# Kernel optimization log

Measured on AMD Instinct MI355X. Metric: run time of the kernel, lower is better.

## Reference

```python
import jax, jax.numpy as jnp
import numpy as np

E = 64      # routed experts
K = 2       # top-k
CAP = 1024


def setup_inputs() -> dict:
    key = jax.random.key(0)
    ks = jax.random.split(key, 5)
    S, B, D, DFF = 2048, 4, 1024, 1408
    x = jax.random.normal(ks[0], (S, B, D), jnp.float32)
    Wg = jax.random.normal(ks[1], (D, E), jnp.float32) * 0.02
    W1 = jax.random.normal(ks[2], (E, D, DFF), jnp.float32) * 0.02
    W3 = jax.random.normal(ks[3], (E, D, DFF), jnp.float32) * 0.02
    W2 = jax.random.normal(ks[4], (E, DFF, D), jnp.float32) * 0.02
    return {"x": x, "Wg": Wg, "W1": W1, "W3": W3, "W2": W2}


def _moe(x, Wg, W1, W3, W2):
    S, B, D = x.shape
    tokens = jnp.transpose(x, (1, 0, 2)).reshape(-1, D)       # [T, D], T = B*S
    T = tokens.shape[0]

    # --- gate: softmax -> top-k, renormalize, aux loss (GShard-style) ---
    logits = tokens @ Wg                                       # [T, E]
    probs = jax.nn.softmax(logits, axis=-1)
    topk_w, topk_idx = jax.lax.top_k(probs, K)                 # [T, K]
    topk_w = topk_w / jnp.sum(topk_w, axis=-1, keepdims=True)
    me = jnp.mean(probs, axis=0)                               # [E] mean prob
    ce = jnp.mean(jax.nn.one_hot(topk_idx, E, dtype=jnp.float32).sum(1), axis=0) / K
    l_aux = E * jnp.sum(me * ce)

    # --- dispatch: per-pair slot within its expert via cumsum of one-hots ---
    flat_e = topk_idx.reshape(-1)                              # [T*K]
    oh = jax.nn.one_hot(flat_e, E, dtype=jnp.int32)            # [T*K, E]
    pos = jnp.cumsum(oh, axis=0) - 1                           # slot per expert
    slot = jnp.take_along_axis(pos, flat_e[:, None], axis=1)[:, 0]  # [T*K]
    keep = slot < CAP
    slot = jnp.where(keep, slot, 0)
    xr = jnp.repeat(tokens, K, axis=0)                         # [T*K, D]
    xr = jnp.where(keep[:, None], xr, 0.0)
    buf = jnp.zeros((E, CAP, D), x.dtype).at[flat_e, slot].add(xr)  # [E, C, D]

    # --- grouped expert FFN: SiLU-gated MLP per expert ---
    h = jax.nn.silu(jnp.einsum('ecd,edf->ecf', buf, W1)) * jnp.einsum('ecd,edf->ecf', buf, W3)
    eo = jnp.einsum('ecf,efd->ecd', h, W2)                     # [E, C, D]

    # --- combine: gather back, weight by gate probs, sum over k ---
    gathered = eo[flat_e, slot] * keep[:, None].astype(x.dtype)  # [T*K, D]
    combined = jnp.sum(gathered.reshape(T, K, D) * topk_w[..., None], axis=1)
    y = jnp.transpose(combined.reshape(B, S, D), (1, 0, 2))    # back to [S, B, D]
    return y, l_aux


def reference(x, Wg, W1, W3, W2):
    return _moe(x, Wg, W1, W3, W2)
```

## Files before the change

kernel.cpp:

```cpp
#include <hip/hip_runtime.h>
#include <hip/hip_bf16.h>


#define S_ 2048
#define B_ 4
#define D_ 1024
#define DFF_ 1408
#define E_ 64
#define T_ 8192
#define KTOP_ 2
#define NPAIR_ (T_*KTOP_)
#define PAD_ 384
#define ROWS_ (E_*PAD_)

#define BM 128
#define BN 64
#define BK 32

typedef __attribute__((ext_vector_type(8))) short short8;
typedef __attribute__((ext_vector_type(4))) short s16x4;
typedef __attribute__((ext_vector_type(4))) float f32x4;
typedef __attribute__((ext_vector_type(4))) unsigned short us4;

constexpr size_t OFF_PROBS  = 0;
constexpr size_t OFF_PE     = OFF_PROBS + (size_t)T_*E_*4;
constexpr size_t OFF_PW     = OFF_PE + (size_t)NPAIR_*4;
constexpr size_t OFF_COUNTS = OFF_PW + (size_t)NPAIR_*4;
constexpr size_t OFF_CURSOR = OFF_COUNTS + 256;
constexpr size_t OFF_MESUM  = OFF_CURSOR + 256;
constexpr size_t OFF_ROWTOK = OFF_MESUM + 256;
constexpr size_t OFF_ROWW   = OFF_ROWTOK + (size_t)ROWS_*4;
constexpr size_t OFF_XBUF   = OFF_ROWW + (size_t)ROWS_*4;
constexpr size_t OFF_H      = OFF_XBUF + (size_t)ROWS_*D_*2;

__device__ __forceinline__ short f2bfs(float f) {
  union { __hip_bfloat16 h; short s; } u;
  u.h = __float2bfloat16(f);
  return u.s;
}

__device__ __forceinline__ int SWZ(int g) { return g ^ (((g >> 4) & 3) << 1); }

#define BAR() do {                                   \
    __builtin_amdgcn_sched_barrier(0);               \
    __builtin_amdgcn_s_barrier();                    \
    __builtin_amdgcn_sched_barrier(0);               \
  } while (0)
#define WAIT_LGKM0() asm volatile("s_waitcnt lgkmcnt(0)" ::: "memory")

__device__ __forceinline__ float softmax64(float acc, int lane) {
  float m = acc;
  for (int o = 32; o; o >>= 1) m = fmaxf(m, __shfl_xor(m, o));
  float p = expf(acc - m);
  float s = p;
  for (int o = 32; o; o >>= 1) s += __shfl_xor(s, o);
  return p / s;
}

__device__ __forceinline__ void topk_write(float p, int t, int lane,
    float* __restrict__ probs, int* __restrict__ pe, float* __restrict__ pw,
    int* __restrict__ counts) {
  probs[(size_t)t * E_ + lane] = p;
  float v1 = p; int i1 = lane;
  for (int o = 32; o; o >>= 1) {
    float ov = __shfl_xor(v1, o); int oi = __shfl_xor(i1, o);
    if (ov > v1 || (ov == v1 && oi < i1)) { v1 = ov; i1 = oi; }
  }
  float v2 = (lane == i1) ? -1.f : p; int i2 = lane;
  for (int o = 32; o; o >>= 1) {
    float ov = __shfl_xor(v2, o); int oi = __shfl_xor(i2, o);
    if (ov > v2 || (ov == v2 && oi < i2)) { v2 = ov; i2 = oi; }
  }
  if (lane == 0) {
    float wsum = v1 + v2;
    pe[2 * t]     = i1; pw[2 * t]     = v1 / wsum;
    pe[2 * t + 1] = i2; pw[2 * t + 1] = v2 / wsum;
    atomicAdd(&counts[i1], 1);
    atomicAdd(&counts[i2], 1);
  }
}

__global__ __launch_bounds__(256) void gate_kernel(
    const float* __restrict__ x, const float* __restrict__ Wg,
    float* __restrict__ probs, int* __restrict__ pe, float* __restrict__ pw,
    int* __restrict__ counts) {
  int t0 = blockIdx.x * 8;
  int tid = threadIdx.x;
  int lane = tid & 63, wv = tid >> 6;
  __shared__ float tk[8][D_];
  for (int u = tid; u < 8 * (D_ / 4); u += 256) {
    int r = u >> 8, c4 = u & 255;
    int t = t0 + r;
    int b = t >> 11, s = t & (S_ - 1);
    ((float4*)tk[r])[c4] = ((const float4*)(x + (size_t)(s * B_ + b) * D_))[c4];
  }
  __syncthreads();
  const float* tkA = tk[2 * wv];
  const float* tkB = tk[2 * wv + 1];
  float acc0 = 0.f, acc1 = 0.f;
  #pragma unroll 8
  for (int d = 0; d < D_; ++d) {
    float w = Wg[(size_t)d * E_ + lane];
    acc0 += tkA[d] * w;
    acc1 += tkB[d] * w;
  }
  int ta = t0 + 2 * wv, tb = ta + 1;
  float p0 = softmax64(acc0, lane);
  float p1 = softmax64(acc1, lane);
  topk_write(p0, ta, lane, probs, pe, pw, counts);
  topk_write(p1, tb, lane, probs, pe, pw, counts);
}

__global__ __launch_bounds__(256) void me_kernel(const float* __restrict__ probs,
                                                 float* __restrict__ mesum) {
  int e = blockIdx.x, tid = threadIdx.x;
  float a = 0.f;
  for (int t = tid; t < T_; t += 256) a += probs[(size_t)t * E_ + e];
  __shared__ float red[256];
  red[tid] = a; __syncthreads();
  for (int s = 128; s; s >>= 1) {
    if (tid < s) red[tid] += red[tid + s];
    __syncthreads();
  }
  if (tid == 0) mesum[e] = red[0];
}

__global__ __launch_bounds__(64) void finalize_kernel(
    const int* __restrict__ counts, const float* __restrict__ mesum,
    float* __restrict__ laux_out) {
  int lane = threadIdx.x;
  float contrib = (mesum[lane] / (float)T_) * ((float)counts[lane] / (float)(T_ * KTOP_));
  for (int o = 32; o; o >>= 1) contrib += __shfl_xor(contrib, o);
  if (lane == 0) laux_out[0] = (float)E_ * contrib;
}

__global__ __launch_bounds__(64) void scatter_kernel(
    const float* __restrict__ x, const int* __restrict__ pe, const float* __restrict__ pw,
    int* __restrict__ cursor, int* __restrict__ rowtok, float* __restrict__ roww,
    unsigned short* __restrict__ xbufO) {
  int p = blockIdx.x;
  int lane = threadIdx.x;
  __shared__ int srow;
  __shared__ int sexp;
  if (lane == 0) {
    int e = pe[p];
    int slot = atomicAdd(&cursor[e], 1);
    int row = (slot < PAD_) ? slot : -1;
    if (row >= 0) { rowtok[e * PAD_ + row] = p >> 1; roww[e * PAD_ + row] = pw[p]; }
    srow = row; sexp = e;
  }
  __syncthreads();
  int m = srow;
  if (m < 0) return;
  int e = sexp;
  int t = p >> 1;
  int b = t >> 11, s = t & (S_ - 1);
  const float4* src = (const float4*)(x + (size_t)(s * B_ + b) * D_);
  unsigned short* dstE = xbufO + (size_t)e * D_ * PAD_;
  #pragma unroll
  for (int oo = 0; oo < 2; ++oo) {
    int o = lane + oo * 64;
    float4 lo = src[o * 2], hi = src[o * 2 + 1];
    short8 g;
    g[0] = f2bfs(lo.x); g[1] = f2bfs(lo.y); g[2] = f2bfs(lo.z); g[3] = f2bfs(lo.w);
    g[4] = f2bfs(hi.x); g[5] = f2bfs(hi.y); g[6] = f2bfs(hi.z); g[7] = f2bfs(hi.w);
    *(short8*)(dstE + ((size_t)o * PAD_ + m) * 8) = g;
  }
}

__global__ __launch_bounds__(256, 3) void ffn1_kernel(
    const unsigned short* __restrict__ xbufO, const float* __restrict__ W1,
    const float* __restrict__ W3, const int* __restrict__ counts,
    unsigned short* __restrict__ hO) {
  int bid = blockIdx.x;
  int r = bid & 7, u = bid >> 3;
  int mb = u % 3; int v = u / 3;
  int ni = v % 22; int eg = v / 22;
  int e = eg * 8 + r;
  int n0 = ni * BN;
  int m0 = mb * BM;
  int Me = min(counts[e], PAD_);
  if (m0 >= Me) return;

  const unsigned short* AO = xbufO + (size_t)e * D_ * PAD_;
  const float* B1p = W1 + (size_t)e * D_ * DFF_ + n0;
  const float* B3p = W3 + (size_t)e * D_ * DFF_ + n0;
  unsigned short* hE = hO + (size_t)e * PAD_ * DFF_;

  __shared__ short B1s[2 * BK * BN];
  __shared__ short B3s[2 * BK * BN];
  __shared__ short Hb[BM * BN];

  int tid = threadIdx.x;
  int lane = tid & 63;
  int wv = tid >> 6, wr = wv >> 1, wc = wv & 1;

  int msel = tid >> 7;
  int t7 = tid & 127;
  int col4 = t7 & 15;
  int krow0 = (t7 >> 4) << 2;
  const float* qB = (msel ? B3p : B1p) + (size_t)krow0 * DFF_ + col4 * 4;
  char* Bdst = (char*)(msel ? B3s : B1s);
  int kseg = krow0 >> 3, khalf8 = ((krow0 >> 2) & 1) << 3;
  int sub = col4 >> 2;
  int boffc[4];
  #pragma unroll
  for (int cc = 0; cc < 4; ++cc)
    boffc[cc] = (sub << 10) + (SWZ((kseg << 4) + ((col4 & 3) * 4 + cc)) << 4) + khalf8;

  const unsigned short* qa =
      AO + (((size_t)(lane >> 4)) * PAD_ + m0 + (wr << 6) + (lane & 15)) * 8;

  short8 afE[4], afO[4];
  f32x4 fBE[4], fBO[4];
  f32x4 acc1[4][2] = {};
  f32x4 acc3[4][2] = {};

#define F1_ALOAD(SET) do {                                               \
    _Pragma("unroll")                                                    \
    for (int mi = 0; mi < 4; ++mi)                                       \
      af##SET[mi] = *(const short8*)(qa + mi * 128);                     \
    qa += (size_t)4 * PAD_ * 8;                                          \
  } while (0)

#define F1_BLOAD(SET) do {                                               \
    _Pragma("unroll")                                                    \
    for (int j = 0; j < 4; ++j)                                          \
      fB##SET[j] = *(const f32x4*)(qB + (size_t)j * DFF_);               \
    qB += (size_t)BK * DFF_;                                             \
  } while (0)

#define F1_BWRITE(SET, BUF) do {                                         \
    _Pragma("unroll")                                                    \
    for (int cc = 0; cc < 4; ++cc) {                                     \
      s16x4 w;                                                           \
      _Pragma("unroll")                                                  \
      for (int j = 0; j < 4; ++j) w[j] = f2bfs(fB##SET[j][cc]);          \
      *(s16x4*)(Bdst + (BUF)*4096 + boffc[cc]) = w;                      \
    }                                                                    \
  } while (0)

#define F1_MFMA(BUF, SET) do {                                           \
    int lsw = SWZ(lane) << 4;                                            \
    __builtin_amdgcn_s_setprio(1);                                       \
    _Pragma("unroll")                                                    \
    for (int q = 0; q < 2; ++q) {                                        \
      short8 bf1 = *(const short8*)((char*)B1s + (BUF)*4096 + (((wc << 1) + q) << 10) + lsw); \
      short8 bf3 = *(const short8*)((char*)B3s + (BUF)*4096 + (((wc << 1) + q) << 10) + lsw); \
      _Pragma("unroll")                                                  \
      for (int mi = 0; mi < 4; ++mi) {                                   \
        acc1[mi][q] = __builtin_amdgcn_mfma_f32_16x16x32_bf16(af##SET[mi], bf1, acc1[mi][q], 0, 0, 0); \
        acc3[mi][q] = __builtin_amdgcn_mfma_f32_16x16x32_bf16(af##SET[mi], bf3, acc3[mi][q], 0, 0, 0); \
      }                                                                  \
    }                                                                    \
    __builtin_amdgcn_s_setprio(0);                                       \
  } while (0)

  F1_ALOAD(E); F1_BLOAD(E);
  F1_ALOAD(O); F1_BLOAD(O);
  for (int it = 0; it < 15; ++it) {
    F1_BWRITE(E, 0); WAIT_LGKM0(); BAR();
    F1_MFMA(0, E);
    BAR();
    F1_ALOAD(E); F1_BLOAD(E);
    F1_BWRITE(O, 1); WAIT_LGKM0(); BAR();
    F1_MFMA(1, O);
    BAR();
    F1_ALOAD(O); F1_BLOAD(O);
  }
  F1_BWRITE(E, 0); WAIT_LGKM0(); BAR(); F1_MFMA(0, E); BAR();
  F1_BWRITE(O, 1); WAIT_LGKM0(); BAR(); F1_MFMA(1, O);

  __syncthreads();
  int lr = (lane >> 4) << 2, lc = lane & 15;
  #pragma unroll
  for (int mi = 0; mi < 4; ++mi) {
    #pragma unroll
    for (int j = 0; j < 4; ++j) {
      int m = ((wr << 2) + mi) * 16 + lr + j;
      #pragma unroll
      for (int q = 0; q < 2; ++q) {
        int c = (wc << 5) + (q << 4) + lc;
        float a = acc1[mi][q][j];
        float gt = a / (1.f + __expf(-a));
        Hb[((c >> 3) * BM + m) * 8 + (c & 7)] = f2bfs(gt * acc3[mi][q][j]);
      }
    }
  }
  __syncthreads();
  int co = tid >> 5, ml0 = (tid & 31) << 2;
  size_t fo = (size_t)(n0 >> 3) + co;
  #pragma unroll
  for (int i = 0; i < 4; ++i) {
    int ml = ml0 + i;
    short8 vq = *(const short8*)(Hb + ((size_t)co * BM + ml) * 8);
    *(short8*)(hE + (fo * PAD_ + m0 + ml) * 8) = vq;
  }
}

__global__ __launch_bounds__(256, 4) void ffn2_kernel(
    const unsigned short* __restrict__ hO, const float* __restrict__ W2,
    const int* __restrict__ counts, const int* __restrict__ rowtok,
    const float* __restrict__ roww, float* __restrict__ y) {
  int bid = blockIdx.x;
  int r = bid & 7, u = bid >> 3;
  int mb = u % 3; int v = u / 3;
  int ni = v % 16; int eg = v / 16;
  int e = eg * 8 + r;
  int n0 = ni * BN;
  int m0 = mb * BM;
  int Me = min(counts[e], PAD_);
  if (m0 >= Me) return;

  const unsigned short* AO = hO + (size_t)e * PAD_ * DFF_;
  const float* Bw = W2 + (size_t)e * DFF_ * D_ + n0;

  __shared__ short Bs[2 * BK * BN];

  int tid = threadIdx.x;
  int lane = tid & 63;
  int wv = tid >> 6, wr = wv >> 1, wc = wv & 1;

  int bstage = (tid < 128);
  int t7 = tid & 127;
  int col4 = t7 & 15;
  int krow0 = (t7 >> 4) << 2;
  const float* qB = Bw + (size_t)krow0 * D_ + col4 * 4;
  int kseg = krow0 >> 3, khalf8 = ((krow0 >> 2) & 1) << 3;
  int sub = col4 >> 2;
  int boffc[4];
  #pragma unroll
  for (int cc = 0; cc < 4; ++cc)
    boffc[cc] = (sub << 10) + (SWZ((kseg << 4) + ((col4 & 3) * 4 + cc)) << 4) + khalf8;

  const unsigned short* qa =
      AO + (((size_t)(lane >> 4)) * PAD_ + m0 + (wr << 6) + (lane & 15)) * 8;

  short8 afE[4], afO[4];
  f32x4 fBE[4], fBO[4];
  f32x4 acc[4][2] = {};

#define F2_ALOAD(SET) do {                                               \
    _Pragma("unroll")                                                    \
    for (int mi = 0; mi < 4; ++mi)                                       \
      af##SET[mi] = *(const short8*)(qa + mi * 128);                     \
    qa += (size_t)4 * PAD_ * 8;                                          \
  } while (0)

#define F2_BLOAD(SET) do {                                               \
    if (bstage) {                                                        \
      _Pragma("unroll")                                                  \
      for (int j = 0; j < 4; ++j)                                        \
        fB##SET[j] = *(const f32x4*)(qB + (size_t)j * D_);               \
    }                                                                    \
    qB += (size_t)BK * D_;                                               \
  } while (0)

#define F2_BWRITE(SET, BUF) do {                                         \
    if (bstage) {                                                        \
      _Pragma("unroll")                                                  \
      for (int cc = 0; cc < 4; ++cc) {                                   \
        s16x4 w;                                                         \
        _Pragma("unroll")                                                \
        for (int j = 0; j < 4; ++j) w[j] = f2bfs(fB##SET[j][cc]);        \
        *(s16x4*)((char*)Bs + (BUF)*4096 + boffc[cc]) = w;               \
      }                                                                  \
    }                                                                    \
  } while (0)

#define F2_MFMA(BUF, SET) do {                                           \
    int lsw = SWZ(lane) << 4;                                            \
    __builtin_amdgcn_s_setprio(1);                                       \
    _Pragma("unroll")                                                    \
    for (int q = 0; q < 2; ++q) {                                        \
      short8 bfr = *(const short8*)((char*)Bs + (BUF)*4096 + (((wc << 1) + q) << 10) + lsw); \
      _Pragma("unroll")                                                  \
      for (int mi = 0; mi < 4; ++mi)                                     \
        acc[mi][q] = __builtin_amdgcn_mfma_f32_16x16x32_bf16(af##SET[mi], bfr, acc[mi][q], 0, 0, 0); \
    }                                                                    \
    __builtin_amdgcn_s_setprio(0);                                       \
  } while (0)

  F2_ALOAD(E); F2_BLOAD(E);
  F2_ALOAD(O); F2_BLOAD(O);
  for (int it = 0; it < 21; ++it) {
    F2_BWRITE(E, 0); WAIT_LGKM0(); BAR();
    F2_MFMA(0, E);
    BAR();
    F2_ALOAD(E); F2_BLOAD(E);
    F2_BWRITE(O, 1); WAIT_LGKM0(); BAR();
    F2_MFMA(1, O);
    BAR();
    F2_ALOAD(O); F2_BLOAD(O);
  }
  F2_BWRITE(E, 0); WAIT_LGKM0(); BAR(); F2_MFMA(0, E); BAR();
  F2_BWRITE(O, 1); WAIT_LGKM0(); BAR(); F2_MFMA(1, O);

  int lr = (lane >> 4) << 2, lc = lane & 15;
  #pragma unroll
  for (int mi = 0; mi < 4; ++mi) {
    #pragma unroll
    for (int j = 0; j < 4; ++j) {
      int m = m0 + ((wr << 2) + mi) * 16 + lr + j;
      if (m < Me) {
        int rw = e * PAD_ + m;
        int t = rowtok[rw];
        float w = roww[rw];
        int b = t >> 11, s = t & (S_ - 1);
        float* yp = y + (size_t)(s * B_ + b) * D_ + n0 + (wc << 5) + lc;
        #pragma unroll
        for (int q = 0; q < 2; ++q)
          atomicAdd(&yp[q << 4], w * acc[mi][q][j]);
      }
    }
  }
}

extern "C" void kernel_launch(void* const* d_in, const int* in_sizes, int n_in,
                              void* d_out, int out_size, void* d_ws, size_t ws_size,
                              hipStream_t stream) {
  const float* x  = (const float*)d_in[0];
  const float* Wg = (const float*)d_in[1];
  const float* W1 = (const float*)d_in[2];
  const float* W3 = (const float*)d_in[3];
  const float* W2 = (const float*)d_in[4];
  float* y = (float*)d_out;
  float* laux = y + (size_t)S_ * B_ * D_;

  char* ws = (char*)d_ws;
  float* probs  = (float*)(ws + OFF_PROBS);
  int*   pe     = (int*)  (ws + OFF_PE);
  float* pw     = (float*)(ws + OFF_PW);
  int*   counts = (int*)  (ws + OFF_COUNTS);
  int*   cursor = (int*)  (ws + OFF_CURSOR);
  float* mesum  = (float*)(ws + OFF_MESUM);
  int*   rowtok = (int*)  (ws + OFF_ROWTOK);
  float* roww   = (float*)(ws + OFF_ROWW);
  unsigned short* xbufO = (unsigned short*)(ws + OFF_XBUF);
  unsigned short* hO    = (unsigned short*)(ws + OFF_H);

  hipMemsetAsync(d_out, 0, (size_t)out_size * sizeof(float), stream);
  hipMemsetAsync(counts, 0, 512, stream);

  gate_kernel<<<T_ / 8, 256, 0, stream>>>(x, Wg, probs, pe, pw, counts);
  me_kernel<<<E_, 256, 0, stream>>>(probs, mesum);
  finalize_kernel<<<1, 64, 0, stream>>>(counts, mesum, laux);
  scatter_kernel<<<NPAIR_, 64, 0, stream>>>(x, pe, pw, cursor, rowtok, roww, xbufO);
  ffn1_kernel<<<8 * 8 * 22 * 3, 256, 0, stream>>>(xbufO, W1, W3, counts, hO);
  ffn2_kernel<<<8 * 8 * 16 * 3, 256, 0, stream>>>(hO, W2, counts, rowtok, roww, y);
}
```

Baseline: 693.5 us.

## Widen FFN GEMM tiles to 128 columns in both expert kernels

Doubles the N tile of the ffn1 and ffn2 grouped GEMMs from 64 to 128 columns, halving the block count and the number of times each expert's activation rows are re-read per output column. The fp32 weight-load mapping, the LDS buffer sizes and offsets, the accumulator arrays and the epilogue are reworked to match. In ffn2 all threads now stage weights instead of half. This costs more registers per thread, so launch bounds drop occupancy targets (3→2 and 4→3), and fewer blocks may underfill the GPU for lightly loaded experts.

```diff
diff --git a/kernel.cpp b/kernel.cpp
--- a/kernel.cpp
+++ b/kernel.cpp
@@ -14,7 +14,7 @@
 #define ROWS_ (E_*PAD_)
 
 #define BM 128
-#define BN 64
+#define BN 128
 #define BK 32
 
 typedef __attribute__((ext_vector_type(8))) short short8;
@@ -168,14 +168,14 @@
   }
 }
 
-__global__ __launch_bounds__(256, 3) void ffn1_kernel(
+__global__ __launch_bounds__(256, 2) void ffn1_kernel(
     const unsigned short* __restrict__ xbufO, const float* __restrict__ W1,
     const float* __restrict__ W3, const int* __restrict__ counts,
     unsigned short* __restrict__ hO) {
   int bid = blockIdx.x;
   int r = bid & 7, u = bid >> 3;
   int mb = u % 3; int v = u / 3;
-  int ni = v % 22; int eg = v / 22;
+  int ni = v % 11; int eg = v / 11;
   int e = eg * 8 + r;
   int n0 = ni * BN;
   int m0 = mb * BM;
@@ -197,24 +197,25 @@
 
   int msel = tid >> 7;
   int t7 = tid & 127;
-  int col4 = t7 & 15;
-  int krow0 = (t7 >> 4) << 2;
+  int col4 = t7 & 31;
+  int krow0 = (t7 >> 5) << 3;
   const float* qB = (msel ? B3p : B1p) + (size_t)krow0 * DFF_ + col4 * 4;
   char* Bdst = (char*)(msel ? B3s : B1s);
-  int kseg = krow0 >> 3, khalf8 = ((krow0 >> 2) & 1) << 3;
-  int sub = col4 >> 2;
+  int kseg = krow0 >> 3;
   int boffc[4];
   #pragma unroll
-  for (int cc = 0; cc < 4; ++cc)
-    boffc[cc] = (sub << 10) + (SWZ((kseg << 4) + ((col4 & 3) * 4 + cc)) << 4) + khalf8;
+  for (int cc = 0; cc < 4; ++cc) {
+    int c = col4 * 4 + cc;
+    boffc[cc] = ((c >> 4) << 10) + (SWZ((kseg << 4) + (c & 15)) << 4);
+  }
 
   const unsigned short* qa =
       AO + (((size_t)(lane >> 4)) * PAD_ + m0 + (wr << 6) + (lane & 15)) * 8;
 
   short8 afE[4], afO[4];
-  f32x4 fBE[4], fBO[4];
-  f32x4 acc1[4][2] = {};
-  f32x4 acc3[4][2] = {};
+  f32x4 fBE[8], fBO[8];
+  f32x4 acc1[4][4] = {};
+  f32x4 acc3[4][4] = {};
 
 #define F1_ALOAD(SET) do {                                               \
     _Pragma("unroll")                                                    \
@@ -225,7 +226,7 @@
 
 #define F1_BLOAD(SET) do {                                               \
     _Pragma("unroll")                                                    \
-    for (int j = 0; j < 4; ++j)                                          \
+    for (int j = 0; j < 8; ++j)                                          \
       fB##SET[j] = *(const f32x4*)(qB + (size_t)j * DFF_);               \
     qB += (size_t)BK * DFF_;                                             \
   } while (0)
@@ -233,10 +234,10 @@
 #define F1_BWRITE(SET, BUF) do {                                         \
     _Pragma("unroll")                                                    \
     for (int cc = 0; cc < 4; ++cc) {                                     \
-      s16x4 w;                                                           \
+      short8 w;                                                          \
       _Pragma("unroll")                                                  \
-      for (int j = 0; j < 4; ++j) w[j] = f2bfs(fB##SET[j][cc]);          \
-      *(s16x4*)(Bdst + (BUF)*4096 + boffc[cc]) = w;                      \
+      for (int j = 0; j < 8; ++j) w[j] = f2bfs(fB##SET[j][cc]);          \
+      *(short8*)(Bdst + (BUF)*8192 + boffc[cc]) = w;                     \
     }                                                                    \
   } while (0)
 
@@ -244,9 +245,9 @@
     int lsw = SWZ(lane) << 4;                                            \
     __builtin_amdgcn_s_setprio(1);                                       \
     _Pragma("unroll")                                                    \
-    for (int q = 0; q < 2; ++q) {                                        \
-      short8 bf1 = *(const short8*)((char*)B1s + (BUF)*4096 + (((wc << 1) + q) << 10) + lsw); \
-      short8 bf3 = *(const short8*)((char*)B3s + (BUF)*4096 + (((wc << 1) + q) << 10) + lsw); \
+    for (int q = 0; q < 4; ++q) {                                        \
+      short8 bf1 = *(const short8*)((char*)B1s + (BUF)*8192 + (((wc << 2) + q) << 10) + lsw); \
+      short8 bf3 = *(const short8*)((char*)B3s + (BUF)*8192 + (((wc << 2) + q) << 10) + lsw); \
       _Pragma("unroll")                                                  \
       for (int mi = 0; mi < 4; ++mi) {                                   \
         acc1[mi][q] = __builtin_amdgcn_mfma_f32_16x16x32_bf16(af##SET[mi], bf1, acc1[mi][q], 0, 0, 0); \
@@ -279,33 +280,33 @@
     for (int j = 0; j < 4; ++j) {
       int m = ((wr << 2) + mi) * 16 + lr + j;
       #pragma unroll
-      for (int q = 0; q < 2; ++q) {
-        int c = (wc << 5) + (q << 4) + lc;
+      for (int q = 0; q < 4; ++q) {
+        int c = (wc << 6) + (q << 4) + lc;
         float a = acc1[mi][q][j];
         float gt = a / (1.f + __expf(-a));
-        Hb[((c >> 3) * BM + m) * 8 + (c & 7)] = f2bfs(gt * acc3[mi][q][j]);
+        Hb[((size_t)(c >> 3) * BM + m) * 8 + (c & 7)] = f2bfs(gt * acc3[mi][q][j]);
       }
     }
   }
   __syncthreads();
-  int co = tid >> 5, ml0 = (tid & 31) << 2;
+  int co = tid >> 4, ml0 = (tid & 15) << 3;
   size_t fo = (size_t)(n0 >> 3) + co;
   #pragma unroll
-  for (int i = 0; i < 4; ++i) {
+  for (int i = 0; i < 8; ++i) {
     int ml = ml0 + i;
     short8 vq = *(const short8*)(Hb + ((size_t)co * BM + ml) * 8);
     *(short8*)(hE + (fo * PAD_ + m0 + ml) * 8) = vq;
   }
 }
 
-__global__ __launch_bounds__(256, 4) void ffn2_kernel(
+__global__ __launch_bounds__(256, 3) void ffn2_kernel(
     const unsigned short* __restrict__ hO, const float* __restrict__ W2,
     const int* __restrict__ counts, const int* __restrict__ rowtok,
     const float* __restrict__ roww, float* __restrict__ y) {
   int bid = blockIdx.x;
   int r = bid & 7, u = bid >> 3;
   int mb = u % 3; int v = u / 3;
-  int ni = v % 16; int eg = v / 16;
+  int ni = v % 8; int eg = v / 8;
   int e = eg * 8 + r;
   int n0 = ni * BN;
   int m0 = mb * BM;
@@ -321,24 +322,23 @@
   int lane = tid & 63;
   int wv = tid >> 6, wr = wv >> 1, wc = wv & 1;
 
-  int bstage = (tid < 128);
-  int t7 = tid & 127;
-  int col4 = t7 & 15;
-  int krow0 = (t7 >> 4) << 2;
+  int col4 = tid & 31;
+  int krow0 = (tid >> 5) << 2;
   const float* qB = Bw + (size_t)krow0 * D_ + col4 * 4;
   int kseg = krow0 >> 3, khalf8 = ((krow0 >> 2) & 1) << 3;
-  int sub = col4 >> 2;
   int boffc[4];
   #pragma unroll
-  for (int cc = 0; cc < 4; ++cc)
-    boffc[cc] = (sub << 10) + (SWZ((kseg << 4) + ((col4 & 3) * 4 + cc)) << 4) + khalf8;
+  for (int cc = 0; cc < 4; ++cc) {
+    int c = col4 * 4 + cc;
+    boffc[cc] = ((c >> 4) << 10) + (SWZ((kseg << 4) + (c & 15)) << 4) + khalf8;
+  }
 
   const unsigned short* qa =
       AO + (((size_t)(lane >> 4)) * PAD_ + m0 + (wr << 6) + (lane & 15)) * 8;
 
   short8 afE[4], afO[4];
   f32x4 fBE[4], fBO[4];
-  f32x4 acc[4][2] = {};
+  f32x4 acc[4][4] = {};
 
 #define F2_ALOAD(SET) do {                                               \
     _Pragma("unroll")                                                    \
@@ -348,23 +348,19 @@
   } while (0)
 
 #define F2_BLOAD(SET) do {                                               \
-    if (bstage) {                                                        \
+    _Pragma("unroll")                                                    \
+    for (int j = 0; j < 4; ++j)                                          \
+      fB##SET[j] = *(const f32x4*)(qB + (size_t)j * D_);                 \
+    qB += (size_t)BK * D_;                                               \
+  } while (0)
+
+#define F2_BWRITE(SET, BUF) do {                                         \
+    _Pragma("unroll")                                                    \
+    for (int cc = 0; cc < 4; ++cc) {                                     \
+      s16x4 w;                                                           \
       _Pragma("unroll")                                                  \
-      for (int j = 0; j < 4; ++j)                                        \
-        fB##SET[j] = *(const f32x4*)(qB + (size_t)j * D_);               \
-    }                                                                    \
-    qB += (size_t)BK * D_;                                               \
-  } while (0)
-
-#define F2_BWRITE(SET, BUF) do {                                         \
-    if (bstage) {                                                        \
-      _Pragma("unroll")                                                  \
-      for (int cc = 0; cc < 4; ++cc) {                                   \
-        s16x4 w;                                                         \
-        _Pragma("unroll")                                                \
-        for (int j = 0; j < 4; ++j) w[j] = f2bfs(fB##SET[j][cc]);        \
-        *(s16x4*)((char*)Bs + (BUF)*4096 + boffc[cc]) = w;               \
-      }                                                                  \
+      for (int j = 0; j < 4; ++j) w[j] = f2bfs(fB##SET[j][cc]);          \
+      *(s16x4*)((char*)Bs + (BUF)*8192 + boffc[cc]) = w;                 \
     }                                                                    \
   } while (0)
 
@@ -372,8 +368,8 @@
     int lsw = SWZ(lane) << 4;                                            \
     __builtin_amdgcn_s_setprio(1);                                       \
     _Pragma("unroll")                                                    \
-    for (int q = 0; q < 2; ++q) {                                        \
-      short8 bfr = *(const short8*)((char*)Bs + (BUF)*4096 + (((wc << 1) + q) << 10) + lsw); \
+    for (int q = 0; q < 4; ++q) {                                        \
+      short8 bfr = *(const short8*)((char*)Bs + (BUF)*8192 + (((wc << 2) + q) << 10) + lsw); \
       _Pragma("unroll")                                                  \
       for (int mi = 0; mi < 4; ++mi)                                     \
         acc[mi][q] = __builtin_amdgcn_mfma_f32_16x16x32_bf16(af##SET[mi], bfr, acc[mi][q], 0, 0, 0); \
@@ -407,9 +403,9 @@
         int t = rowtok[rw];
         float w = roww[rw];
         int b = t >> 11, s = t & (S_ - 1);
-        float* yp = y + (size_t)(s * B_ + b) * D_ + n0 + (wc << 5) + lc;
+        float* yp = y + (size_t)(s * B_ + b) * D_ + n0 + (wc << 6) + lc;
         #pragma unroll
-        for (int q = 0; q < 2; ++q)
+        for (int q = 0; q < 4; ++q)
           atomicAdd(&yp[q << 4], w * acc[mi][q][j]);
       }
     }
@@ -446,6 +442,6 @@
   me_kernel<<<E_, 256, 0, stream>>>(probs, mesum);
   finalize_kernel<<<1, 64, 0, stream>>>(counts, mesum, laux);
   scatter_kernel<<<NPAIR_, 64, 0, stream>>>(x, pe, pw, cursor, rowtok, roww, xbufO);
-  ffn1_kernel<<<8 * 8 * 22 * 3, 256, 0, stream>>>(xbufO, W1, W3, counts, hO);
-  ffn2_kernel<<<8 * 8 * 16 * 3, 256, 0, stream>>>(hO, W2, counts, rowtok, roww, y);
-}
+  ffn1_kernel<<<8 * 8 * 11 * 3, 256, 0, stream>>>(xbufO, W1, W3, counts, hO);
+  ffn2_kernel<<<8 * 8 * 8 * 3, 256, 0, stream>>>(hO, W2, counts, rowtok, roww, y);
+}
```

After: 651.5 us. 1.06x faster.
